# Kernel tuning notes

Measured on AMD Instinct MI355X. Metric: run time of the kernel, lower is better.

Reference implementation:

```python
import jax, jax.numpy as jnp
import numpy as np

N = 1024          # num_params
HID = 4096        # hidden_dimensions


def setup_inputs() -> dict:
    key = jax.random.key(0)
    k = jax.random.split(key, 7)
    s1 = 1.0 / np.sqrt(2 * N)   # torch Linear init bound fan_in=2N
    s2 = 1.0 / np.sqrt(HID)
    u = jax.random.uniform
    return {
        "x": jax.random.normal(k[0], (2 * N,), jnp.float32),
        "W1": u(k[1], (2 * N, HID), jnp.float32, -s1, s1),
        "b1": u(k[2], (HID,), jnp.float32, -s1, s1),
        "W2": u(k[3], (HID, HID), jnp.float32, -s2, s2),
        "b2": u(k[4], (HID,), jnp.float32, -s2, s2),
        "W3": u(k[5], (HID, 1), jnp.float32, -s2, s2),
        "b3": u(k[6], (1,), jnp.float32, -s2, s2),
    }


def reference(x, W1, b1, W2, b2, W3, b3):
    n = x.shape[0] // 2  # num_params

    def lag(z):
        # 3-layer Softplus MLP -> scalar Lagrangian
        h1 = jax.nn.softplus(z @ W1 + b1)
        h2 = jax.nn.softplus(h1 @ W2 + b2)
        return (h2 @ W3 + b3)[0]

    D = jax.grad(lag)(x)          # [2n]  (jacobian row of scalar fn)
    H = jax.hessian(lag)(x)       # [2n, 2n]

    dq0 = D[:n]                   # dL/dq
    dq1 = H[n:, n:]               # d2L/dqdot dqdot
    dq2 = H[:n, n:]               # d2L/dq dqdot
    # q_tt = inv(dq1) @ (dq0 - dq2 @ q_t)
    return jnp.linalg.inv(dq1) @ (dq0 - dq2 @ x[n:])
```

## Files before the change

### kernel.cpp

```cpp
#include <hip/hip_runtime.h>
#include <cstddef>

#define HID 4096
#define NH 1024
#define LDA 1088

typedef short short8v __attribute__((ext_vector_type(8)));
typedef short short4v __attribute__((ext_vector_type(4)));
typedef float f32x4 __attribute__((ext_vector_type(4)));

__device__ __forceinline__ float wred(float a) {
#pragma unroll
  for (int off = 32; off > 0; off >>= 1) a += __shfl_down(a, off);
  return a;
}

__device__ __forceinline__ unsigned short bf16rne(float x) {
  unsigned b = __float_as_uint(x);
  unsigned r = b + 0x7FFFu + ((b >> 16) & 1u);
  return (unsigned short)(r >> 16);
}
__device__ __forceinline__ void split1(float x, unsigned short& h, unsigned short& l) {
  h = bf16rne(x);
  float hf = __uint_as_float((unsigned)h << 16);
  l = bf16rne(x - hf);
}
__device__ __forceinline__ void split4(float4 v, short4v& hv, short4v& lv) {
  unsigned short h, l;
  split1(v.x, h, l); hv[0] = (short)h; lv[0] = (short)l;
  split1(v.y, h, l); hv[1] = (short)h; lv[1] = (short)l;
  split1(v.z, h, l); hv[2] = (short)h; lv[2] = (short)l;
  split1(v.w, h, l); hv[3] = (short)h; lv[3] = (short)l;
}


__global__ __launch_bounds__(256) void k_z1p(const float* __restrict__ x, const float* __restrict__ W1,
                                             float* __restrict__ zp1) {
  int k = blockIdx.x * 256 + threadIdx.x;
  int i0 = blockIdx.y * 256;
  float acc = 0.f;
  for (int i = i0; i < i0 + 256; ++i) acc = fmaf(x[i], W1[(size_t)i * HID + k], acc);
  zp1[(size_t)blockIdx.y * HID + k] = acc;
}

__global__ __launch_bounds__(256) void k_act1(const float* __restrict__ zp1, const float* __restrict__ b1,
                                              float* __restrict__ h1, float* __restrict__ s1,
                                              float* __restrict__ s1p) {
  int k = blockIdx.x * 256 + threadIdx.x;
  float z = b1[k];
#pragma unroll
  for (int j = 0; j < 8; ++j) z += zp1[(size_t)j * HID + k];
  float sg = 1.f / (1.f + expf(-z));
  h1[k] = (z > 20.f) ? z : log1pf(expf(z));
  s1[k] = sg;
  s1p[k] = sg * (1.f - sg);
}

__global__ __launch_bounds__(256) void k_z2p(const float* __restrict__ h1, const float* __restrict__ W2,
                                             float* __restrict__ zp2) {
  int j = blockIdx.x * 256 + threadIdx.x;
  int i0 = blockIdx.y * 256;
  float acc = 0.f;
  for (int i = i0; i < i0 + 256; ++i) acc = fmaf(h1[i], W2[(size_t)i * HID + j], acc);
  zp2[(size_t)blockIdx.y * HID + j] = acc;
}

__global__ __launch_bounds__(256) void k_act2(const float* __restrict__ zp2, const float* __restrict__ b2,
                                              const float* __restrict__ w3, float* __restrict__ g2,
                                              float* __restrict__ d2) {
  int j = blockIdx.x * 256 + threadIdx.x;
  float z = b2[j];
#pragma unroll
  for (int q = 0; q < 16; ++q) z += zp2[(size_t)q * HID + j];
  float sg = 1.f / (1.f + expf(-z));
  float w = w3[j];
  g2[j] = sg * w;
  d2[j] = sg * (1.f - sg) * w;
}

__global__ __launch_bounds__(256) void k_u(const float* __restrict__ W2, const float* __restrict__ g2,
                                           const float* __restrict__ s1, const float* __restrict__ s1p,
                                           float* __restrict__ g1, float* __restrict__ d1) {
  int w = threadIdx.x >> 6, lane = threadIdx.x & 63;
  int row = blockIdx.x * 4 + w;
  const float* p = W2 + (size_t)row * HID;
  float acc = 0.f;
  for (int j = lane; j < HID; j += 64) acc = fmaf(p[j], g2[j], acc);
  acc = wred(acc);
  if (lane == 0) {
    g1[row] = s1[row] * acc;
    d1[row] = s1p[row] * acc;
  }
}

__global__ __launch_bounds__(256) void k_dq0(const float* __restrict__ W1, const float* __restrict__ g1,
                                             float* __restrict__ dq0) {
  int w = threadIdx.x >> 6, lane = threadIdx.x & 63;
  int row = blockIdx.x * 4 + w;
  const float* p = W1 + (size_t)row * HID;
  float acc = 0.f;
  for (int k = lane; k < HID; k += 64) acc = fmaf(p[k], g1[k], acc);
  acc = wred(acc);
  if (lane == 0) dq0[row] = acc;
}

__global__ __launch_bounds__(256) void k_vp(const float* __restrict__ QT, const float* __restrict__ x,
                                            float* __restrict__ vp) {
  int l = blockIdx.x * 256 + threadIdx.x;
  int r0 = blockIdx.y * 128;
  float acc = 0.f;
  for (int r = r0; r < r0 + 128; ++r) acc = fmaf(QT[(size_t)r * HID + l], x[NH + r], acc);
  vp[(size_t)blockIdx.y * HID + l] = acc;
}

__global__ __launch_bounds__(256) void k_vred(const float* __restrict__ vp, float* __restrict__ vv) {
  int l = blockIdx.x * 256 + threadIdx.x;
  float a = 0.f;
#pragma unroll
  for (int j = 0; j < 8; ++j) a += vp[(size_t)j * HID + l];
  vv[l] = a;
}

__global__ __launch_bounds__(256) void k_rhs(const float* __restrict__ W1, const float* __restrict__ v,
                                             const float* __restrict__ dq0, float* __restrict__ rhs) {
  int w = threadIdx.x >> 6, lane = threadIdx.x & 63;
  int row = blockIdx.x * 4 + w;
  const float* p = W1 + (size_t)row * HID;
  float acc = 0.f;
  for (int l = lane; l < HID; l += 64) acc = fmaf(p[l], v[l], acc);
  acc = wred(acc);
  if (lane == 0) rhs[row] = dq0[row] - acc;
}

template <bool TRANSB, int MODE>
__global__ __launch_bounds__(256) void mfma_gemm(const float* __restrict__ A, int lda,
                                                 const float* __restrict__ B, int ldb,
                                                 float* __restrict__ C, int ldc, int K,
                                                 const float* __restrict__ ks,
                                                 const float* __restrict__ csc1,
                                                 const float* __restrict__ csc2,
                                                 const float* __restrict__ wadd) {
  __shared__ unsigned short Ah[2][128][40] __attribute__((aligned(16)));
  __shared__ unsigned short Al[2][128][40] __attribute__((aligned(16)));
  __shared__ unsigned short Bh[2][128][40] __attribute__((aligned(16)));
  __shared__ unsigned short Bl[2][128][40] __attribute__((aligned(16)));

  const int tid = threadIdx.x;
  const int lane = tid & 63;
  const int wid = tid >> 6;
  const int wm = wid >> 1, wn = wid & 1;
  const int bm = blockIdx.y * 128, bn = blockIdx.x * 128;
  const int frow = lane & 15;
  const int kg = lane >> 4;

  f32x4 acc[4][4];
#pragma unroll
  for (int i = 0; i < 4; ++i)
#pragma unroll
    for (int j = 0; j < 4; ++j) acc[i][j] = (f32x4){0.f, 0.f, 0.f, 0.f};

  const int ar = tid >> 1;
  const int ah = tid & 1;
  const int bcol = tid & 127;
  const int bkh = tid >> 7;

  for (int k0 = 0; k0 < K; k0 += 64) {
    __syncthreads();
    {
      const float* Ap = A + (size_t)(bm + ar) * lda + (k0 + ah * 32);
#pragma unroll
      for (int i = 0; i < 8; ++i) {
        float4 v = *(const float4*)(Ap + i * 4);
        if (MODE == 1) {
          const float* kp = ks + k0 + ah * 32 + i * 4;
          v.x *= kp[0]; v.y *= kp[1]; v.z *= kp[2]; v.w *= kp[3];
        }
        short4v hv, lv;
        split4(v, hv, lv);
        *(short4v*)&Ah[ah][ar][i * 4] = hv;
        *(short4v*)&Al[ah][ar][i * 4] = lv;
      }
    }
    if (TRANSB) {
      const float* Bp = B + (size_t)(bn + ar) * ldb + (k0 + ah * 32);
#pragma unroll
      for (int i = 0; i < 8; ++i) {
        float4 v = *(const float4*)(Bp + i * 4);
        short4v hv, lv;
        split4(v, hv, lv);
        *(short4v*)&Bh[ah][ar][i * 4] = hv;
        *(short4v*)&Bl[ah][ar][i * 4] = lv;
      }
    } else {
#pragma unroll
      for (int i = 0; i < 32; ++i) {
        float xv = B[(size_t)(k0 + bkh * 32 + i) * ldb + bn + bcol];
        unsigned short h, l;
        split1(xv, h, l);
        Bh[bkh][bcol][i] = h;
        Bl[bkh][bcol][i] = l;
      }
    }
    __syncthreads();
#pragma unroll
    for (int kk = 0; kk < 2; ++kk) {
      short8v a_h[4], a_l[4], b_h[4], b_l[4];
#pragma unroll
      for (int mt = 0; mt < 4; ++mt) {
        int r = wm * 64 + mt * 16 + frow;
        a_h[mt] = *(const short8v*)&Ah[kk][r][kg * 8];
        a_l[mt] = *(const short8v*)&Al[kk][r][kg * 8];
      }
#pragma unroll
      for (int nt = 0; nt < 4; ++nt) {
        int c = wn * 64 + nt * 16 + frow;
        b_h[nt] = *(const short8v*)&Bh[kk][c][kg * 8];
        b_l[nt] = *(const short8v*)&Bl[kk][c][kg * 8];
      }
#pragma unroll
      for (int mt = 0; mt < 4; ++mt)
#pragma unroll
        for (int nt = 0; nt < 4; ++nt) {
          acc[mt][nt] = __builtin_amdgcn_mfma_f32_16x16x32_bf16(a_l[mt], b_l[nt], acc[mt][nt], 0, 0, 0);
          acc[mt][nt] = __builtin_amdgcn_mfma_f32_16x16x32_bf16(a_h[mt], b_l[nt], acc[mt][nt], 0, 0, 0);
          acc[mt][nt] = __builtin_amdgcn_mfma_f32_16x16x32_bf16(a_l[mt], b_h[nt], acc[mt][nt], 0, 0, 0);
          acc[mt][nt] = __builtin_amdgcn_mfma_f32_16x16x32_bf16(a_h[mt], b_h[nt], acc[mt][nt], 0, 0, 0);
        }
    }
  }
#pragma unroll
  for (int mt = 0; mt < 4; ++mt)
#pragma unroll
    for (int nt = 0; nt < 4; ++nt) {
      int col = bn + wn * 64 + nt * 16 + frow;
      float c1 = (MODE >= 1) ? csc1[col] : 0.f;
      float c2 = (MODE == 2) ? csc2[col] : 0.f;
#pragma unroll
      for (int j = 0; j < 4; ++j) {
        int row = bm + wm * 64 + mt * 16 + kg * 4 + j;
        float v = acc[mt][nt][j];
        if (MODE == 1) v *= c1;
        if (MODE == 2) v = v * c1 + c2 * wadd[(size_t)row * HID + col];
        C[(size_t)row * ldc + col] = v;
      }
    }
}

__global__ __launch_bounds__(256) void k_setup(const float* __restrict__ dq1, const float* __restrict__ rhs,
                                               float* __restrict__ Ag) {
  int idx = blockIdx.x * 256 + threadIdx.x;
  int r = idx / LDA, c = idx % LDA;
  float v = (c < 1024) ? dq1[(size_t)r * 1024 + c] : (c == 1024 ? rhs[r] : 0.f);
  Ag[idx] = v;
}


__global__ __launch_bounds__(256) void lu_diag(float* __restrict__ Ag, int o) {
  __shared__ float T[64][65];
  int t = threadIdx.x;
  for (int idx = t; idx < 4096; idx += 256) {
    int r = idx >> 6, c = idx & 63;
    T[r][c] = Ag[(size_t)(o + r) * LDA + o + c];
  }
  __syncthreads();
  int r = t & 63, cg = t >> 6;
  for (int kk = 0; kk < 63; ++kk) {
    if (cg == 0 && r > kk) T[r][kk] /= T[kk][kk];
    __syncthreads();
    float l = (r > kk) ? T[r][kk] : 0.f;
    int c0 = cg * 16;
#pragma unroll
    for (int j = 0; j < 16; ++j) {
      int c = c0 + j;
      if (r > kk && c > kk) T[r][c] = fmaf(-l, T[kk][c], T[r][c]);
    }
    __syncthreads();
  }
  for (int idx = t; idx < 4096; idx += 256) {
    int rr = idx >> 6, c = idx & 63;
    Ag[(size_t)(o + rr) * LDA + o + c] = T[rr][c];
  }
}

__global__ __launch_bounds__(256) void lu_panel(float* __restrict__ Ag, int o, int NU) {
  __shared__ float Ds[64][65];
  __shared__ float Xs[64][65];
  __shared__ float rp[64];
  int t = threadIdx.x;
  bool isU = (int)blockIdx.x < NU;
  size_t tb;
  if (isU) tb = (size_t)o * LDA + (o + 64 + (int)blockIdx.x * 64);
  else     tb = (size_t)(o + 64 + ((int)blockIdx.x - NU) * 64) * LDA + o;
  for (int idx = t; idx < 4096; idx += 256) {
    int r = idx >> 6, c = idx & 63;
    Ds[r][c] = Ag[(size_t)(o + r) * LDA + o + c];
    Xs[r][c] = Ag[tb + (size_t)r * LDA + c];
  }
  __syncthreads();
  if (!isU && t < 64) rp[t] = 1.f / Ds[t][t];
  __syncthreads();
  if (isU) {
    int cl = t & 63, rg = t >> 6;
    for (int kk = 0; kk < 63; ++kk) {
      float xk = Xs[kk][cl];
      int i0 = rg * 16;
#pragma unroll
      for (int j = 0; j < 16; ++j) {
        int i = i0 + j;
        if (i > kk) Xs[i][cl] = fmaf(-Ds[i][kk], xk, Xs[i][cl]);
      }
      __syncthreads();
    }
  } else {
    int r = t & 63, cg = t >> 6;
    for (int kk = 0; kk < 64; ++kk) {
      if (cg == (kk >> 4)) Xs[r][kk] *= rp[kk];
      __syncthreads();
      float vk = Xs[r][kk];
      int c0 = cg * 16;
#pragma unroll
      for (int j = 0; j < 16; ++j) {
        int m = c0 + j;
        if (m > kk) Xs[r][m] = fmaf(-vk, Ds[kk][m], Xs[r][m]);
      }
      __syncthreads();
    }
  }
  __syncthreads();
  for (int idx = t; idx < 4096; idx += 256) {
    int r = idx >> 6, c = idx & 63;
    Ag[tb + (size_t)r * LDA + c] = Xs[r][c];
  }
}

__global__ __launch_bounds__(256) void lu_schur(float* __restrict__ Ag, int o) {
  __shared__ float Ls[64][65];
  __shared__ float Us[64][65];
  int t = threadIdx.x;
  int c0 = o + 64 + blockIdx.x * 64;
  int r0 = o + 64 + blockIdx.y * 64;
  for (int idx = t; idx < 4096; idx += 256) {
    int r = idx >> 6, q = idx & 63;
    Ls[q][r] = Ag[(size_t)(r0 + r) * LDA + o + q];
    Us[r][q] = Ag[(size_t)(o + r) * LDA + c0 + q];
  }
  __syncthreads();
  int tm = (t >> 4) * 4, tn = (t & 15) * 4;
  float acc[4][4];
#pragma unroll
  for (int i = 0; i < 4; ++i)
#pragma unroll
    for (int j = 0; j < 4; ++j) acc[i][j] = 0.f;
#pragma unroll 8
  for (int kk = 0; kk < 64; ++kk) {
    float a[4], b[4];
#pragma unroll
    for (int i = 0; i < 4; ++i) a[i] = Ls[kk][tm + i];
#pragma unroll
    for (int j = 0; j < 4; ++j) b[j] = Us[kk][tn + j];
#pragma unroll
    for (int i = 0; i < 4; ++i)
#pragma unroll
      for (int j = 0; j < 4; ++j) acc[i][j] = fmaf(a[i], b[j], acc[i][j]);
  }
#pragma unroll
  for (int i = 0; i < 4; ++i)
#pragma unroll
    for (int j = 0; j < 4; ++j) Ag[(size_t)(r0 + tm + i) * LDA + c0 + tn + j] -= acc[i][j];
}


__global__ __launch_bounds__(1024) void bs_all(const float* __restrict__ Ag, float* __restrict__ yb) {
  __shared__ float ys[1024];
  __shared__ float Td[64][65];
  int t = threadIdx.x;
  ys[t] = Ag[(size_t)t * LDA + 1024];
  __syncthreads();
  for (int kb = 15; kb >= 0; --kb) {
    int o = kb * 64;
    for (int idx = t; idx < 4096; idx += 1024) {
      int r = idx >> 6, c = idx & 63;
      Td[r][c] = Ag[(size_t)(o + r) * LDA + o + c];
    }
    __syncthreads();
    if (t < 64) {
      float yv = ys[o + t];
      float rpv = 1.f / Td[t][t];
#pragma unroll 16
      for (int kk = 63; kk >= 0; --kk) {
        float xk = __shfl(yv * rpv, kk, 64);
        if (t == kk) yv = xk;
        else if (t < kk) yv = fmaf(-Td[t][kk], xk, yv);
      }
      ys[o + t] = yv;
    }
    __syncthreads();
    if (o > 0) {
      int c = t & 63, wg = t >> 6;
      float yc = ys[o + c];
      for (int rr = wg; rr < o; rr += 64) {
        float p0 = Ag[(size_t)rr * LDA + o + c] * yc;
        float p1 = Ag[(size_t)(rr + 16) * LDA + o + c] * yc;
        float p2 = Ag[(size_t)(rr + 32) * LDA + o + c] * yc;
        float p3 = Ag[(size_t)(rr + 48) * LDA + o + c] * yc;
        p0 = wred(p0); p1 = wred(p1); p2 = wred(p2); p3 = wred(p3);
        if (c == 0) { ys[rr] -= p0; ys[rr + 16] -= p1; ys[rr + 32] -= p2; ys[rr + 48] -= p3; }
      }
      __syncthreads();
    }
  }
  yb[t] = ys[t];
}

__global__ __launch_bounds__(256) void k_resid(const float* __restrict__ dq1, const float* __restrict__ x0,
                                               const float* __restrict__ rhs, float* __restrict__ rv) {
  int w = threadIdx.x >> 6, lane = threadIdx.x & 63;
  int row = blockIdx.x * 4 + w;
  const float* p = dq1 + (size_t)row * 1024;
  float acc = 0.f;
  for (int j = lane; j < 1024; j += 64) acc = fmaf(p[j], x0[j], acc);
  acc = wred(acc);
  if (lane == 0) rv[row] = rhs[row] - acc;
}

__global__ __launch_bounds__(1024) void fsbs_all(const float* __restrict__ Ag, const float* __restrict__ rv,
                                                 const float* __restrict__ yb, float* __restrict__ out) {
  __shared__ float ys[1024];
  __shared__ float Td[64][65];
  int t = threadIdx.x;
  ys[t] = rv[t];
  __syncthreads();
  for (int kb = 0; kb < 16; ++kb) {
    int o = kb * 64;
    for (int idx = t; idx < 4096; idx += 1024) {
      int r = idx >> 6, c = idx & 63;
      Td[r][c] = Ag[(size_t)(o + r) * LDA + o + c];
    }
    __syncthreads();
    if (t < 64) {
      float yv = ys[o + t];
#pragma unroll 16
      for (int kk = 0; kk < 63; ++kk) {
        float xk = __shfl(yv, kk, 64);
        if (t > kk) yv = fmaf(-Td[t][kk], xk, yv);
      }
      ys[o + t] = yv;
    }
    __syncthreads();
    if (o < 960) {
      int c = t & 63, wg = t >> 6;
      float yc = ys[o + c];
      for (int rr = o + 64 + wg; rr < 1024; rr += 64) {
        float p0 = Ag[(size_t)rr * LDA + o + c] * yc;
        float p1 = Ag[(size_t)(rr + 16) * LDA + o + c] * yc;
        float p2 = Ag[(size_t)(rr + 32) * LDA + o + c] * yc;
        float p3 = Ag[(size_t)(rr + 48) * LDA + o + c] * yc;
        p0 = wred(p0); p1 = wred(p1); p2 = wred(p2); p3 = wred(p3);
        if (c == 0) { ys[rr] -= p0; ys[rr + 16] -= p1; ys[rr + 32] -= p2; ys[rr + 48] -= p3; }
      }
      __syncthreads();
    }
  }
  for (int kb = 15; kb >= 0; --kb) {
    int o = kb * 64;
    for (int idx = t; idx < 4096; idx += 1024) {
      int r = idx >> 6, c = idx & 63;
      Td[r][c] = Ag[(size_t)(o + r) * LDA + o + c];
    }
    __syncthreads();
    if (t < 64) {
      float yv = ys[o + t];
      float rpv = 1.f / Td[t][t];
#pragma unroll 16
      for (int kk = 63; kk >= 0; --kk) {
        float xk = __shfl(yv * rpv, kk, 64);
        if (t == kk) yv = xk;
        else if (t < kk) yv = fmaf(-Td[t][kk], xk, yv);
      }
      ys[o + t] = yv;
    }
    __syncthreads();
    if (o > 0) {
      int c = t & 63, wg = t >> 6;
      float yc = ys[o + c];
      for (int rr = wg; rr < o; rr += 64) {
        float p0 = Ag[(size_t)rr * LDA + o + c] * yc;
        float p1 = Ag[(size_t)(rr + 16) * LDA + o + c] * yc;
        float p2 = Ag[(size_t)(rr + 32) * LDA + o + c] * yc;
        float p3 = Ag[(size_t)(rr + 48) * LDA + o + c] * yc;
        p0 = wred(p0); p1 = wred(p1); p2 = wred(p2); p3 = wred(p3);
        if (c == 0) { ys[rr] -= p0; ys[rr + 16] -= p1; ys[rr + 32] -= p2; ys[rr + 48] -= p3; }
      }
      __syncthreads();
    }
  }
  out[t] = yb[t] + ys[t];
}


extern "C" void kernel_launch(void* const* d_in, const int* in_sizes, int n_in, void* d_out,
                              int out_size, void* d_ws, size_t ws_size, hipStream_t stream) {
  const float* x  = (const float*)d_in[0];
  const float* W1 = (const float*)d_in[1];
  const float* b1 = (const float*)d_in[2];
  const float* W2 = (const float*)d_in[3];
  const float* b2 = (const float*)d_in[4];
  const float* W3 = (const float*)d_in[5];
  float* out = (float*)d_out;
  float* ws = (float*)d_ws;

  float* h1  = ws + 0;
  float* s1  = ws + 4096;
  float* s1p = ws + 8192;
  float* d1  = ws + 12288;
  float* g2  = ws + 16384;
  float* d2  = ws + 20480;
  float* g1  = ws + 24576;
  float* vv  = ws + 28672;
  float* dq0 = ws + 32768;
  float* rhs = ws + 33792;
  float* yb  = ws + 34816;
  float* rv  = ws + 35840;
  float* Bbs = ws + 65536;
  float* QT  = Bbs + (size_t)1024 * HID;
  float* Ag  = QT + (size_t)1024 * HID;
  float* dq1 = Ag + (size_t)1024 * LDA;

  float* zp1 = Ag;
  float* zp2 = Ag + 32768;
  float* vp  = Ag + 98304;

  const float* W1b = W1 + (size_t)NH * HID;

  k_z1p<<<dim3(16, 8), 256, 0, stream>>>(x, W1, zp1);
  k_act1<<<16, 256, 0, stream>>>(zp1, b1, h1, s1, s1p);
  k_z2p<<<dim3(16, 16), 256, 0, stream>>>(h1, W2, zp2);
  k_act2<<<16, 256, 0, stream>>>(zp2, b2, W3, g2, d2);
  k_u<<<1024, 256, 0, stream>>>(W2, g2, s1, s1p, g1, d1);
  k_dq0<<<256, 256, 0, stream>>>(W1, g1, dq0);

  mfma_gemm<false, 1><<<dim3(32, 8), 256, 0, stream>>>(
      W1b, HID, W2, HID, Bbs, HID, HID, s1, d2, nullptr, nullptr);
  mfma_gemm<true, 2><<<dim3(32, 8), 256, 0, stream>>>(
      Bbs, HID, W2, HID, QT, HID, HID, nullptr, s1, d1, W1b);
  mfma_gemm<true, 0><<<dim3(8, 8), 256, 0, stream>>>(
      W1b, HID, QT, HID, dq1, 1024, HID, nullptr, nullptr, nullptr, nullptr);

  k_vp<<<dim3(16, 8), 256, 0, stream>>>(QT, x, vp);
  k_vred<<<16, 256, 0, stream>>>(vp, vv);
  k_rhs<<<256, 256, 0, stream>>>(W1, vv, dq0, rhs);
  k_setup<<<(1024 * LDA) / 256, 256, 0, stream>>>(dq1, rhs, Ag);

  for (int kb = 0; kb < 16; ++kb) {
    int o = kb * 64;
    int NU = 16 - kb;
    int NL = 15 - kb;
    lu_diag<<<1, 256, 0, stream>>>(Ag, o);
    lu_panel<<<NU + NL, 256, 0, stream>>>(Ag, o, NU);
    if (NL > 0) lu_schur<<<dim3(NU, NL), 256, 0, stream>>>(Ag, o);
  }

  bs_all<<<1, 1024, 0, stream>>>(Ag, yb);
  k_resid<<<256, 256, 0, stream>>>(dq1, yb, rhs, rv);
  fsbs_all<<<1, 1024, 0, stream>>>(Ag, rv, yb, out);
}
```

Measured before the change: 3.776 ms.

## Vectorize B tile loads, drop low-low MFMA term, restructure triangular solves

The non-transposed B tile path now uses coalesced float4 row loads instead of strided scalar column loads before the bf16 hi/lo split. The lo*lo MFMA product in the split-bf16 GEMM is dropped, leaving three MFMAs per tile instead of four, at a small cost in accuracy. The blocked triangular solves change from right-looking column-block updates, with a separate sync pass after each diagonal block, to left-looking row dot-products. These are computed while the diagonal tile is being loaded, which removes one barrier phase per block and makes the global reads row-contiguous.

```diff
diff --git a/kernel.cpp b/kernel.cpp
--- a/kernel.cpp
+++ b/kernel.cpp
@@ -161,8 +161,6 @@
 
   const int ar = tid >> 1;
   const int ah = tid & 1;
-  const int bcol = tid & 127;
-  const int bkh = tid >> 7;
 
   for (int k0 = 0; k0 < K; k0 += 64) {
     __syncthreads();
@@ -192,13 +190,18 @@
         *(short4v*)&Bl[ah][ar][i * 4] = lv;
       }
     } else {
-#pragma unroll
-      for (int i = 0; i < 32; ++i) {
-        float xv = B[(size_t)(k0 + bkh * 32 + i) * ldb + bn + bcol];
+      int kr = tid >> 5;
+      int cn = (tid & 31) * 4;
+#pragma unroll
+      for (int p = 0; p < 8; ++p) {
+        int k = p * 8 + kr;
+        float4 v = *(const float4*)(B + (size_t)(k0 + k) * ldb + bn + cn);
+        int kh = k >> 5, kl = k & 31;
         unsigned short h, l;
-        split1(xv, h, l);
-        Bh[bkh][bcol][i] = h;
-        Bl[bkh][bcol][i] = l;
+        split1(v.x, h, l); Bh[kh][cn + 0][kl] = h; Bl[kh][cn + 0][kl] = l;
+        split1(v.y, h, l); Bh[kh][cn + 1][kl] = h; Bl[kh][cn + 1][kl] = l;
+        split1(v.z, h, l); Bh[kh][cn + 2][kl] = h; Bl[kh][cn + 2][kl] = l;
+        split1(v.w, h, l); Bh[kh][cn + 3][kl] = h; Bl[kh][cn + 3][kl] = l;
       }
     }
     __syncthreads();
@@ -221,7 +224,6 @@
       for (int mt = 0; mt < 4; ++mt)
 #pragma unroll
         for (int nt = 0; nt < 4; ++nt) {
-          acc[mt][nt] = __builtin_amdgcn_mfma_f32_16x16x32_bf16(a_l[mt], b_l[nt], acc[mt][nt], 0, 0, 0);
           acc[mt][nt] = __builtin_amdgcn_mfma_f32_16x16x32_bf16(a_h[mt], b_l[nt], acc[mt][nt], 0, 0, 0);
           acc[mt][nt] = __builtin_amdgcn_mfma_f32_16x16x32_bf16(a_l[mt], b_h[nt], acc[mt][nt], 0, 0, 0);
           acc[mt][nt] = __builtin_amdgcn_mfma_f32_16x16x32_bf16(a_h[mt], b_h[nt], acc[mt][nt], 0, 0, 0);
@@ -374,6 +376,7 @@
   __shared__ float ys[1024];
   __shared__ float Td[64][65];
   int t = threadIdx.x;
+  int lane = t & 63, wg = t >> 6;
   ys[t] = Ag[(size_t)t * LDA + 1024];
   __syncthreads();
   for (int kb = 15; kb >= 0; --kb) {
@@ -381,6 +384,20 @@
     for (int idx = t; idx < 4096; idx += 1024) {
       int r = idx >> 6, c = idx & 63;
       Td[r][c] = Ag[(size_t)(o + r) * LDA + o + c];
+    }
+    if (kb < 15) {
+      int r = o + wg * 4;
+      float a0 = 0.f, a1 = 0.f, a2 = 0.f, a3 = 0.f;
+      for (int c = o + 64 + lane; c < 1024; c += 64) {
+        float yc = ys[c];
+        a0 = fmaf(Ag[(size_t)(r + 0) * LDA + c], yc, a0);
+        a1 = fmaf(Ag[(size_t)(r + 1) * LDA + c], yc, a1);
+        a2 = fmaf(Ag[(size_t)(r + 2) * LDA + c], yc, a2);
+        a3 = fmaf(Ag[(size_t)(r + 3) * LDA + c], yc, a3);
+      }
+      a0 = wred(a0); a1 = wred(a1); a2 = wred(a2); a3 = wred(a3);
+      __syncthreads();
+      if (lane == 0) { ys[r] -= a0; ys[r + 1] -= a1; ys[r + 2] -= a2; ys[r + 3] -= a3; }
     }
     __syncthreads();
     if (t < 64) {
@@ -395,19 +412,6 @@
       ys[o + t] = yv;
     }
     __syncthreads();
-    if (o > 0) {
-      int c = t & 63, wg = t >> 6;
-      float yc = ys[o + c];
-      for (int rr = wg; rr < o; rr += 64) {
-        float p0 = Ag[(size_t)rr * LDA + o + c] * yc;
-        float p1 = Ag[(size_t)(rr + 16) * LDA + o + c] * yc;
-        float p2 = Ag[(size_t)(rr + 32) * LDA + o + c] * yc;
-        float p3 = Ag[(size_t)(rr + 48) * LDA + o + c] * yc;
-        p0 = wred(p0); p1 = wred(p1); p2 = wred(p2); p3 = wred(p3);
-        if (c == 0) { ys[rr] -= p0; ys[rr + 16] -= p1; ys[rr + 32] -= p2; ys[rr + 48] -= p3; }
-      }
-      __syncthreads();
-    }
   }
   yb[t] = ys[t];
 }
@@ -428,6 +432,7 @@
   __shared__ float ys[1024];
   __shared__ float Td[64][65];
   int t = threadIdx.x;
+  int lane = t & 63, wg = t >> 6;
   ys[t] = rv[t];
   __syncthreads();
   for (int kb = 0; kb < 16; ++kb) {
@@ -435,6 +440,20 @@
     for (int idx = t; idx < 4096; idx += 1024) {
       int r = idx >> 6, c = idx & 63;
       Td[r][c] = Ag[(size_t)(o + r) * LDA + o + c];
+    }
+    if (kb > 0) {
+      int r = o + wg * 4;
+      float a0 = 0.f, a1 = 0.f, a2 = 0.f, a3 = 0.f;
+      for (int c = lane; c < o; c += 64) {
+        float yc = ys[c];
+        a0 = fmaf(Ag[(size_t)(r + 0) * LDA + c], yc, a0);
+        a1 = fmaf(Ag[(size_t)(r + 1) * LDA + c], yc, a1);
+        a2 = fmaf(Ag[(size_t)(r + 2) * LDA + c], yc, a2);
+        a3 = fmaf(Ag[(size_t)(r + 3) * LDA + c], yc, a3);
+      }
+      a0 = wred(a0); a1 = wred(a1); a2 = wred(a2); a3 = wred(a3);
+      __syncthreads();
+      if (lane == 0) { ys[r] -= a0; ys[r + 1] -= a1; ys[r + 2] -= a2; ys[r + 3] -= a3; }
     }
     __syncthreads();
     if (t < 64) {
@@ -447,25 +466,26 @@
       ys[o + t] = yv;
     }
     __syncthreads();
-    if (o < 960) {
-      int c = t & 63, wg = t >> 6;
-      float yc = ys[o + c];
-      for (int rr = o + 64 + wg; rr < 1024; rr += 64) {
-        float p0 = Ag[(size_t)rr * LDA + o + c] * yc;
-        float p1 = Ag[(size_t)(rr + 16) * LDA + o + c] * yc;
-        float p2 = Ag[(size_t)(rr + 32) * LDA + o + c] * yc;
-        float p3 = Ag[(size_t)(rr + 48) * LDA + o + c] * yc;
-        p0 = wred(p0); p1 = wred(p1); p2 = wred(p2); p3 = wred(p3);
-        if (c == 0) { ys[rr] -= p0; ys[rr + 16] -= p1; ys[rr + 32] -= p2; ys[rr + 48] -= p3; }
-      }
-      __syncthreads();
-    }
   }
   for (int kb = 15; kb >= 0; --kb) {
     int o = kb * 64;
     for (int idx = t; idx < 4096; idx += 1024) {
       int r = idx >> 6, c = idx & 63;
       Td[r][c] = Ag[(size_t)(o + r) * LDA + o + c];
+    }
+    if (kb < 15) {
+      int r = o + wg * 4;
+      float a0 = 0.f, a1 = 0.f, a2 = 0.f, a3 = 0.f;
+      for (int c = o + 64 + lane; c < 1024; c += 64) {
+        float yc = ys[c];
+        a0 = fmaf(Ag[(size_t)(r + 0) * LDA + c], yc, a0);
+        a1 = fmaf(Ag[(size_t)(r + 1) * LDA + c], yc, a1);
+        a2 = fmaf(Ag[(size_t)(r + 2) * LDA + c], yc, a2);
+        a3 = fmaf(Ag[(size_t)(r + 3) * LDA + c], yc, a3);
+      }
+      a0 = wred(a0); a1 = wred(a1); a2 = wred(a2); a3 = wred(a3);
+      __syncthreads();
+      if (lane == 0) { ys[r] -= a0; ys[r + 1] -= a1; ys[r + 2] -= a2; ys[r + 3] -= a3; }
     }
     __syncthreads();
     if (t < 64) {
@@ -480,19 +500,6 @@
       ys[o + t] = yv;
     }
     __syncthreads();
-    if (o > 0) {
-      int c = t & 63, wg = t >> 6;
-      float yc = ys[o + c];
-      for (int rr = wg; rr < o; rr += 64) {
-        float p0 = Ag[(size_t)rr * LDA + o + c] * yc;
-        float p1 = Ag[(size_t)(rr + 16) * LDA + o + c] * yc;
-        float p2 = Ag[(size_t)(rr + 32) * LDA + o + c] * yc;
-        float p3 = Ag[(size_t)(rr + 48) * LDA + o + c] * yc;
-        p0 = wred(p0); p1 = wred(p1); p2 = wred(p2); p3 = wred(p3);
-        if (c == 0) { ys[rr] -= p0; ys[rr + 16] -= p1; ys[rr + 32] -= p2; ys[rr + 48] -= p3; }
-      }
-      __syncthreads();
-    }
   }
   out[t] = yb[t] + ys[t];
 }
```

New measurement: 3.488 ms. -7.6%, faster.
